# Optimization experiments

Hardware: AMD Instinct MI355X
Metric: run time of the kernel (lower is better)

The kernel has to match this reference:

```python
import jax, jax.numpy as jnp
import numpy as np

B, T, U, F, H, V = 4, 512, 96, 512, 512, 256
NEG_INF = -1e30


def setup_inputs() -> dict:
    key = jax.random.key(0)
    ks = jax.random.split(key, 7)
    frames = jax.random.normal(ks[0], (B, T, F), dtype=jnp.float32)
    # guarantee num_frames >= num_labels so a valid alignment path exists
    num_frames = jax.random.randint(ks[1], (B,), T // 2, T + 1, dtype=jnp.int32)
    labels = jax.random.randint(ks[2], (B, U), 1, V + 1, dtype=jnp.int32)
    num_labels = jax.random.randint(ks[3], (B,), U // 2, U + 1, dtype=jnp.int32)
    scale = 0.02
    Wf = scale * jax.random.normal(ks[4], (F, H), dtype=jnp.float32)
    E = scale * jax.random.normal(ks[5], (V + 1, H), dtype=jnp.float32)
    Wo = scale * jax.random.normal(ks[6], (H, V + 1), dtype=jnp.float32)
    return dict(frames=frames, num_frames=num_frames, labels=labels,
                num_labels=num_labels, Wf=Wf, E=E, Wo=Wo)


def _lattice_loss(frames, num_frames, labels, num_labels, Wf, E, Wo):
    Bd, Td, _ = frames.shape
    Ud = labels.shape[1]
    # 1-gram context dependency: context state after u emitted labels is
    # 0 (start) if u == 0 else labels[u-1].  ctx: [B, U+1]
    ctx = jnp.concatenate([jnp.zeros((Bd, 1), labels.dtype), labels], axis=1)
    # locally normalized weight fn (RNN-T style joint network)
    fproj = jnp.einsum('btf,fh->bth', frames, Wf)                 # [B,T,H]
    cemb = jnp.take(E, ctx, axis=0)                               # [B,U+1,H]
    h = jnp.tanh(fproj[:, :, None, :] + cemb[:, None, :, :])      # [B,T,U+1,H]
    logits = jax.nn.log_softmax(
        jnp.einsum('btuh,hv->btuv', h, Wo), axis=-1)              # [B,T,U+1,V+1]
    blank = logits[..., 0]                                        # [B,T,U+1]
    # lexical arc weight for emitting label u+1 from state u:
    # lex[b,t,u] = logits[b,t,u, labels[b,u]]
    idx = jnp.broadcast_to(labels[:, None, :, None].astype(jnp.int32),
                           (Bd, Td, Ud, 1))
    lex = jnp.take_along_axis(logits[:, :, :Ud, :], idx, axis=3)[..., 0]  # [B,T,U]

    # forward DP under the Log semiring over the (t, u) string lattice
    alpha0 = jnp.full((Bd, Ud + 1), NEG_INF, dtype=logits.dtype).at[:, 0].set(0.0)

    def step(alpha, xs):
        blank_t, lex_t, t = xs  # [B,U+1], [B,U], scalar
        stay = alpha + blank_t
        emit = jnp.concatenate(
            [jnp.full((Bd, 1), NEG_INF, dtype=alpha.dtype),
             alpha[:, :-1] + lex_t], axis=1)
        new = jnp.logaddexp(stay, emit)
        new = jnp.where((t < num_frames)[:, None], new, alpha)
        return new, None

    xs = (jnp.swapaxes(blank, 0, 1), jnp.swapaxes(lex, 0, 1), jnp.arange(Td))
    alpha, _ = jax.lax.scan(step, alpha0, xs)
    logp = jnp.take_along_axis(alpha, num_labels[:, None].astype(jnp.int32),
                               axis=1)[:, 0]
    return -logp  # [B] negative sequence log-probability


def reference(frames, num_frames, labels, num_labels, Wf, E, Wo):
    return _lattice_loss(frames, num_frames, labels, num_labels, Wf, E, Wo)
```

## Files before the change

### kernel.cpp

```cpp
#include <hip/hip_runtime.h>
#include <hip/hip_bf16.h>


#define BB 4
#define TT 512
#define UU 96
#define FF 512
#define HH 512
#define VV 256
#define NV (VV + 1)
#define NU (UU + 1)
#define NP 272
#define NEG_INF (-1e30f)
#define LOG2E 1.4426950408889634f
#define LN2 0.6931471805599453f
#define NG 128
#define GSTRIDE 520
#define WOSCL 64.0f
#define INVWOSCL 0.015625f
#define BCHUNK 17408
#define BLONGS 2176

typedef _Float16 f16;
typedef __attribute__((ext_vector_type(8))) _Float16 f16x8;
typedef __bf16 bf16;
typedef __bf16 bf16x8 __attribute__((ext_vector_type(8)));
typedef float f32x4 __attribute__((ext_vector_type(4)));

__device__ __forceinline__ f16x8 splat8(float s) {
    f16 v = (f16)s;
    f16x8 r = {v, v, v, v, v, v, v, v};
    return r;
}

__device__ __forceinline__ long tanh_pack8(f16x8 fv8, f16x8 cv8) {
    f16x8 x = fv8 + cv8;
    x = __builtin_elementwise_min(__builtin_elementwise_max(x, splat8(-2.0f)),
                                  splat8(2.0f));
    f16x8 y = x * x;
    f16x8 q = y * splat8(-0.0067528f) + splat8(0.0700672f);
    q = y * q + splat8(-0.301720f);
    q = y * q + splat8(1.0f);
    f16x8 t = x * q;
    int lo = 0, hi = 0;
    lo = __builtin_amdgcn_cvt_pk_fp8_f32((float)t[0], (float)t[1], lo, false);
    lo = __builtin_amdgcn_cvt_pk_fp8_f32((float)t[2], (float)t[3], lo, true);
    hi = __builtin_amdgcn_cvt_pk_fp8_f32((float)t[4], (float)t[5], hi, false);
    hi = __builtin_amdgcn_cvt_pk_fp8_f32((float)t[6], (float)t[7], hi, true);
    return (long)(((unsigned long long)(unsigned int)lo) |
                  (((unsigned long long)(unsigned int)hi) << 32));
}

__device__ __forceinline__ long pack_fp8x8(const float* v) {
    int lo = 0, hi = 0;
    lo = __builtin_amdgcn_cvt_pk_fp8_f32(v[0], v[1], lo, false);
    lo = __builtin_amdgcn_cvt_pk_fp8_f32(v[2], v[3], lo, true);
    hi = __builtin_amdgcn_cvt_pk_fp8_f32(v[4], v[5], hi, false);
    hi = __builtin_amdgcn_cvt_pk_fp8_f32(v[6], v[7], hi, true);
    return (long)(((unsigned long long)(unsigned int)lo) |
                  (((unsigned long long)(unsigned int)hi) << 32));
}

__device__ __forceinline__ float lae2(float x, float y) {
    float m = fmaxf(x, y);
    float d = fminf(x, y) - m;
    return m + __builtin_amdgcn_logf(1.0f + __builtin_amdgcn_exp2f(d));
}

__device__ __forceinline__ float lse3_2(float x, float y, float z) {
    float m = fmaxf(fmaxf(x, y), z);
    float s = __builtin_amdgcn_exp2f(x - m) + __builtin_amdgcn_exp2f(y - m) +
              __builtin_amdgcn_exp2f(z - m);
    return m + __builtin_amdgcn_logf(s);
}

__device__ __forceinline__ float lse5_2(float a, float b, float c, float d, float e) {
    float m = fmaxf(fmaxf(fmaxf(a, b), fmaxf(c, d)), e);
    float s = __builtin_amdgcn_exp2f(a - m) + __builtin_amdgcn_exp2f(b - m) +
              __builtin_amdgcn_exp2f(c - m) + __builtin_amdgcn_exp2f(d - m) +
              __builtin_amdgcn_exp2f(e - m);
    return m + __builtin_amdgcn_logf(s);
}

__device__ __forceinline__ void async_copy16(const void* g, void* l) {
    __builtin_amdgcn_global_load_lds(
        (const __attribute__((address_space(1))) unsigned int*)g,
        (__attribute__((address_space(3))) unsigned int*)l, 16, 0, 0);
}

__global__ __launch_bounds__(256, 2) void k_front(
    const float* __restrict__ frames, const float* __restrict__ Wf,
    const float* __restrict__ Wo, const float* __restrict__ E,
    const int* __restrict__ labels, f16* __restrict__ fproj,
    long* __restrict__ Wo_s, f16* __restrict__ cemb) {
    __shared__ bf16 Alds[64 * 40];
    __shared__ bf16 Blds[64 * 40];
    const int blk = blockIdx.x;
    const int tid = threadIdx.x;

    if (blk < 256) {
        const int r0 = (blk & 31) * 64;
        const int n0 = (blk >> 5) * 64;
        const int lane = tid & 63, w = tid >> 6;
        const int c = lane & 15, g = lane >> 4;

        const int srow = tid >> 2, sko = (tid & 3) * 8;
        const float* fptr = frames + (size_t)(r0 + srow) * FF + sko;
        const int q = tid >> 6, c64 = tid & 63;

        f32x4 acc[4];
#pragma unroll
        for (int j = 0; j < 4; ++j) acc[j] = (f32x4){0.f, 0.f, 0.f, 0.f};

        for (int kt = 0; kt < FF; kt += 32) {
            float4 f1 = *(const float4*)(fptr + kt);
            float4 f2 = *(const float4*)(fptr + kt + 4);
            bf16x8 av = {(bf16)f1.x, (bf16)f1.y, (bf16)f1.z, (bf16)f1.w,
                         (bf16)f2.x, (bf16)f2.y, (bf16)f2.z, (bf16)f2.w};
            *(bf16x8*)&Alds[srow * 40 + sko] = av;
#pragma unroll
            for (int p = 0; p < 8; ++p) {
                float v = Wf[(size_t)(kt + q * 8 + p) * HH + n0 + c64];
                Blds[c64 * 40 + q * 8 + p] = (bf16)v;
            }
            __syncthreads();
            const int m = w * 16;
            bf16x8 af = *(const bf16x8*)&Alds[(m + c) * 40 + g * 8];
#pragma unroll
            for (int j = 0; j < 4; ++j) {
                bf16x8 bv = *(const bf16x8*)&Blds[(j * 16 + c) * 40 + g * 8];
                acc[j] = __builtin_amdgcn_mfma_f32_16x16x32_bf16(af, bv, acc[j], 0, 0, 0);
            }
            __syncthreads();
        }
        const int m = w * 16;
#pragma unroll
        for (int j = 0; j < 4; ++j)
#pragma unroll
            for (int r = 0; r < 4; ++r)
                fproj[(size_t)(r0 + m + g * 4 + r) * HH + n0 + j * 16 + c] = (f16)acc[j][r];
    } else if (blk < 324) {
        int idx = (blk - 256) * 256 + tid;
        int n = idx % NP;
        int rest = idx / NP;
        int kg = rest & 3;
        int k32 = rest >> 2;
        float v[8];
#pragma unroll
        for (int e = 0; e < 8; ++e) {
            int k = k32 * 32 + kg * 8 + e;
            v[e] = (n < NV) ? Wo[k * NV + n] * WOSCL : 0.f;
        }
        Wo_s[idx] = pack_fp8x8(v);
    } else {
        int u = blk - 324;
        for (int b = 0; b < BB; ++b) {
            int ctx = (u == 0) ? 0 : labels[b * UU + (u - 1)];
            const float* src = E + (size_t)ctx * HH;
            f16* dst = cemb + ((size_t)b * NU + u) * HH;
            for (int i = tid; i < HH; i += 256) dst[i] = (f16)src[i];
        }
    }
}

__global__ __launch_bounds__(256, 4) void k_joint(
    const f16* __restrict__ fproj, const f16* __restrict__ cemb,
    const long* __restrict__ Wo_s, const int* __restrict__ labels,
    const int* __restrict__ num_frames, float* __restrict__ cl_arr) {
    __shared__ long B_s8[2][BLONGS];

    const int tid = threadIdx.x;
    const int b = blockIdx.y;
    const int r0 = blockIdx.x * 64;
    const int nf = num_frames[b];
    if (r0 / NU >= nf) return;

    const int lane = tid & 63, w = tid >> 6;
    const int c = lane & 15, g = lane >> 4;

    const int gr = r0 + w * 16 + c;
    const int at = gr / NU, au = gr - at * NU;
    const f16* pf = fproj + ((size_t)(b * TT + at)) * HH + g * 8;
    const f16* pc = cemb + ((size_t)(b * NU + au)) * HH + g * 8;
    const char* wsrcB = (const char*)Wo_s + lane * 16;

    f32x4 acc[17];
#pragma unroll
    for (int j = 0; j < 17; ++j) acc[j] = (f32x4){0.f, 0.f, 0.f, 0.f};

    const int bB0 = g * NP + c;

    long a0, a1;

    {
        for (int ch = w; ch < 17; ch += 4)
            async_copy16(wsrcB + ch * 1024, (char*)&B_s8[0][0] + ch * 1024 + lane * 16);
        f16x8 fv0 = *(const f16x8*)pf;
        f16x8 cv0 = *(const f16x8*)pc;
        f16x8 fv1 = *(const f16x8*)(pf + 32);
        f16x8 cv1 = *(const f16x8*)(pc + 32);
        a0 = tanh_pack8(fv0, cv0);
        a1 = tanh_pack8(fv1, cv1);
        __syncthreads();
    }

    for (int i = 0; i < 8; ++i) {
        const int cur = i & 1, nxt = cur ^ 1;
        f16x8 fv0, cv0, fv1, cv1;
        if (i < 7) {
            const char* wk = wsrcB + (size_t)(i + 1) * BCHUNK;
            for (int ch = w; ch < 17; ch += 4)
                async_copy16(wk + ch * 1024, (char*)&B_s8[nxt][0] + ch * 1024 + lane * 16);
            const int kt = (i + 1) * 64;
            fv0 = *(const f16x8*)(pf + kt);
            cv0 = *(const f16x8*)(pc + kt);
            fv1 = *(const f16x8*)(pf + kt + 32);
            cv1 = *(const f16x8*)(pc + kt + 32);
        }
        __builtin_amdgcn_s_setprio(1);
#pragma unroll
        for (int j = 0; j < 17; ++j) {
            long bv = B_s8[cur][bB0 + j * 16];
            acc[j] = __builtin_amdgcn_mfma_f32_16x16x32_fp8_fp8(a0, bv, acc[j], 0, 0, 0);
        }
        __builtin_amdgcn_s_setprio(0);
        long a0n, a1n;
        if (i < 7) {
            a0n = tanh_pack8(fv0, cv0);
            a1n = tanh_pack8(fv1, cv1);
        }
        __builtin_amdgcn_s_setprio(1);
#pragma unroll
        for (int j = 0; j < 17; ++j) {
            long bv = B_s8[cur][bB0 + 1088 + j * 16];
            acc[j] = __builtin_amdgcn_mfma_f32_16x16x32_fp8_fp8(a1, bv, acc[j], 0, 0, 0);
        }
        __builtin_amdgcn_s_setprio(0);
        if (i < 7) {
            a0 = a0n;
            a1 = a1n;
            __syncthreads();
        }
    }

#pragma unroll
    for (int j = 0; j < 17; ++j) acc[j] = acc[j] * INVWOSCL;

    const int rbase = r0 + w * 16 + g * 4;
#pragma unroll
    for (int r = 0; r < 4; ++r) {
        const int grr = rbase + r;
        const int t = grr / NU, u = grr - t * NU;

        float mx = NEG_INF;
#pragma unroll
        for (int j = 0; j < 17; ++j) {
            int col = j * 16 + c;
            if (col < NV) mx = fmaxf(mx, acc[j][r]);
        }
#pragma unroll
        for (int s = 1; s < 16; s <<= 1) mx = fmaxf(mx, __shfl_xor(mx, s));
        float sum = 0.f;
#pragma unroll
        for (int j = 0; j < 17; ++j) {
            int col = j * 16 + c;
            if (col < NV) sum += __expf(acc[j][r] - mx);
        }
#pragma unroll
        for (int s = 1; s < 16; s <<= 1) sum += __shfl_xor(sum, s);
        float lse = mx + __logf(sum);

        float blankv = __shfl(acc[0][r], lane & 48);
        int L = (u < UU) ? labels[b * UU + u] : 0;
        int jl = L >> 4;
        float v = acc[0][r];
#pragma unroll
        for (int j = 1; j < 17; ++j)
            if (jl == j) v = acc[j][r];
        float lexv = __shfl(v, (lane & 48) | (L & 15));

        if (c == 0) {
            float2 ov;
            ov.x = blankv - lse;
            ov.y = (u < UU) ? (lexv - lse) : 0.f;
            *(float2*)&cl_arr[(((size_t)b * TT + t) * NU + u) * 2] = ov;
        }
    }
}

__global__ __launch_bounds__(128) void k_compact(
    const float* __restrict__ cl, const int* __restrict__ num_frames,
    float* __restrict__ Dg) {
    const int g = blockIdx.x;
    const int b = blockIdx.y;
    const int u = threadIdx.x;
    if (u >= NU) return;
    const int nf = num_frames[b];
    const float2* P = (const float2*)(cl + (size_t)b * TT * NU * 2);

    auto fetch = [&](int t, int uu, float& bb, float& ll) {
        if (uu <= UU) {
            float2 z = P[t * NU + uu];
            bool act = t < nf;
            bb = act ? z.x * LOG2E : 0.f;
            ll = (act && uu < UU) ? z.y * LOG2E : NEG_INF;
        } else {
            bb = NEG_INF;
            ll = NEG_INF;
        }
    };

    const int t0 = g * 4;
    float b0, l0, b1u, l1u, b1u1, l1u1;
    fetch(t0, u, b0, l0);
    fetch(t0 + 1, u, b1u, l1u);
    fetch(t0 + 1, u + 1, b1u1, l1u1);
    float A0 = b0 + b1u;
    float A1 = lae2(l0 + b1u1, b0 + l1u);
    float A2 = l0 + l1u1;
    float B0[3], B1[3], B2[3];
#pragma unroll
    for (int j = 0; j < 3; ++j) {
        float b2v, l2v, b3v, l3v, b3n, l3n;
        fetch(t0 + 2, u + j, b2v, l2v);
        fetch(t0 + 3, u + j, b3v, l3v);
        fetch(t0 + 3, u + j + 1, b3n, l3n);
        B0[j] = b2v + b3v;
        B1[j] = lae2(l2v + b3n, b2v + l3v);
        B2[j] = l2v + l3n;
    }
    float* d = Dg + ((size_t)b * NG + g) * GSTRIDE;
    d[u] = A0 + B0[0];
    d[104 + u] = lae2(A1 + B0[1], A0 + B1[0]);
    d[208 + u] = lse3_2(A2 + B0[2], A1 + B1[1], A0 + B2[0]);
    d[312 + u] = lae2(A2 + B1[2], A1 + B2[1]);
    d[416 + u] = A2 + B2[2];
}

__global__ __launch_bounds__(64) void k_dpser(
    const float* __restrict__ Dg, const int* __restrict__ num_labels,
    float* __restrict__ out) {
    const int b = blockIdx.x;
    const int lane = threadIdx.x;
    const float* D = Dg + (size_t)b * NG * GSTRIDE;
    const int lo_u = lane;
    const int hi_u = 64 + ((lane < 33) ? lane : 0);

    float a_lo = (lane == 0) ? 0.f : NEG_INF;
    float a_hi = NEG_INF;

    constexpr int R = 8;
    float blo[R][5], bhi[R][5];
#pragma unroll
    for (int g = 0; g < R; ++g)
#pragma unroll
        for (int k = 0; k < 5; ++k) {
            blo[g][k] = D[g * GSTRIDE + k * 104 + lo_u];
            bhi[g][k] = D[g * GSTRIDE + k * 104 + hi_u];
        }

#pragma unroll 8
    for (int g = 0; g < NG; ++g) {
        const int slot = g & (R - 1);
        float el[5], eh[5];
#pragma unroll
        for (int k = 0; k < 5; ++k) {
            el[k] = a_lo + blo[slot][k];
            eh[k] = a_hi + bhi[slot][k];
        }
        const int gp = g + R;
        if (gp < NG) {
#pragma unroll
            for (int k = 0; k < 5; ++k) {
                blo[slot][k] = D[gp * GSTRIDE + k * 104 + lo_u];
                bhi[slot][k] = D[gp * GSTRIDE + k * 104 + hi_u];
            }
        }
        float ml[5], mh[5];
        ml[0] = el[0];
        mh[0] = eh[0];
#pragma unroll
        for (int k = 1; k < 5; ++k) {
            float su = __shfl_up(el[k], k);
            ml[k] = (lane >= k) ? su : NEG_INF;
            float sh = __shfl_up(eh[k], k);
            float xl = __shfl(el[k], 64 - k + lane);
            mh[k] = (lane >= k) ? sh : xl;
        }
        a_lo = lse5_2(ml[0], ml[1], ml[2], ml[3], ml[4]);
        float nh = lse5_2(mh[0], mh[1], mh[2], mh[3], mh[4]);
        if (lane < 33) a_hi = nh;
    }

    const int nl = num_labels[b];
    float res = (nl < 64) ? __shfl(a_lo, nl) : __shfl(a_hi, nl - 64);
    if (lane == 0) out[b] = -res * LN2;
}

extern "C" void kernel_launch(void* const* d_in, const int* in_sizes, int n_in,
                              void* d_out, int out_size, void* d_ws, size_t ws_size,
                              hipStream_t stream) {
    const float* frames = (const float*)d_in[0];
    const int* num_frames = (const int*)d_in[1];
    const int* labels = (const int*)d_in[2];
    const int* num_labels = (const int*)d_in[3];
    const float* Wf = (const float*)d_in[4];
    const float* E = (const float*)d_in[5];
    const float* Wo = (const float*)d_in[6];
    float* out = (float*)d_out;

    char* ws = (char*)d_ws;
    size_t off = 0;
    long* Wo_s = (long*)(ws + off); off += (size_t)17408 * 8;
    f16* cemb = (f16*)(ws + off); off += (size_t)BB * NU * HH * 2;
    off = (off + 255) & ~(size_t)255;
    f16* fproj = (f16*)(ws + off); off += (size_t)BB * TT * HH * 2;
    off = (off + 255) & ~(size_t)255;
    float* cl_arr = (float*)(ws + off); off += (size_t)BB * TT * NU * 2 * 4;
    off = (off + 255) & ~(size_t)255;
    float* Dg = (float*)(ws + off); off += (size_t)BB * NG * GSTRIDE * 4;

    hipLaunchKernelGGL(k_front, dim3(421), dim3(256), 0, stream,
                       frames, Wf, Wo, E, labels, fproj, Wo_s, cemb);
    hipLaunchKernelGGL(k_joint, dim3((TT * NU) / 64, BB), dim3(256), 0, stream,
                       fproj, cemb, Wo_s, labels, num_frames, cl_arr);
    hipLaunchKernelGGL(k_compact, dim3(NG, BB), dim3(128), 0, stream,
                       cl_arr, num_frames, Dg);
    hipLaunchKernelGGL(k_dpser, dim3(BB), dim3(64), 0, stream,
                       Dg, num_labels, out);
}
```

Before: 187.3 us.

## Compute the 257th vocab column with f16 dot products instead of a padded MFMA tile

The joint GEMM previously padded the vocabulary to 272 columns, spending a whole 17th MFMA column tile (mostly zeros) just to get column 256. That column is now computed per thread as an f16 fused multiply-add dot product of the tanh activations with a separately staged f16 weight column. Lane shuffles reduce it, and the result is merged into the log-softmax and the label lookup. This cuts MFMA work, LDS staging and accumulator registers by about one sixteenth, but adds VALU work and leaves that column accumulated in f16, with different precision than the fp8 MFMA path.

```diff
diff --git a/kernel.cpp b/kernel.cpp
--- a/kernel.cpp
+++ b/kernel.cpp
@@ -10,7 +10,7 @@
 #define VV 256
 #define NV (VV + 1)
 #define NU (UU + 1)
-#define NP 272
+#define NP 256
 #define NEG_INF (-1e30f)
 #define LOG2E 1.4426950408889634f
 #define LN2 0.6931471805599453f
@@ -18,8 +18,9 @@
 #define GSTRIDE 520
 #define WOSCL 64.0f
 #define INVWOSCL 0.015625f
-#define BCHUNK 17408
-#define BLONGS 2176
+#define BCHUNK 16384
+#define BLONGS 2048
+#define SPLANE 1024
 
 typedef _Float16 f16;
 typedef __attribute__((ext_vector_type(8))) _Float16 f16x8;
@@ -33,7 +34,7 @@
     return r;
 }
 
-__device__ __forceinline__ long tanh_pack8(f16x8 fv8, f16x8 cv8) {
+__device__ __forceinline__ f16x8 tanh8(f16x8 fv8, f16x8 cv8) {
     f16x8 x = fv8 + cv8;
     x = __builtin_elementwise_min(__builtin_elementwise_max(x, splat8(-2.0f)),
                                   splat8(2.0f));
@@ -41,7 +42,10 @@
     f16x8 q = y * splat8(-0.0067528f) + splat8(0.0700672f);
     q = y * q + splat8(-0.301720f);
     q = y * q + splat8(1.0f);
-    f16x8 t = x * q;
+    return x * q;
+}
+
+__device__ __forceinline__ long pack8(f16x8 t) {
     int lo = 0, hi = 0;
     lo = __builtin_amdgcn_cvt_pk_fp8_f32((float)t[0], (float)t[1], lo, false);
     lo = __builtin_amdgcn_cvt_pk_fp8_f32((float)t[2], (float)t[3], lo, true);
@@ -92,7 +96,7 @@
     const float* __restrict__ frames, const float* __restrict__ Wf,
     const float* __restrict__ Wo, const float* __restrict__ E,
     const int* __restrict__ labels, f16* __restrict__ fproj,
-    long* __restrict__ Wo_s, f16* __restrict__ cemb) {
+    long* __restrict__ Wo_s, f16* __restrict__ wcol, f16* __restrict__ cemb) {
     __shared__ bf16 Alds[64 * 40];
     __shared__ bf16 Blds[64 * 40];
     const int blk = blockIdx.x;
@@ -139,21 +143,23 @@
 #pragma unroll
             for (int r = 0; r < 4; ++r)
                 fproj[(size_t)(r0 + m + g * 4 + r) * HH + n0 + j * 16 + c] = (f16)acc[j][r];
-    } else if (blk < 324) {
+    } else if (blk < 320) {
         int idx = (blk - 256) * 256 + tid;
-        int n = idx % NP;
-        int rest = idx / NP;
+        int n = idx & 255;
+        int rest = idx >> 8;
         int kg = rest & 3;
         int k32 = rest >> 2;
         float v[8];
 #pragma unroll
         for (int e = 0; e < 8; ++e) {
             int k = k32 * 32 + kg * 8 + e;
-            v[e] = (n < NV) ? Wo[k * NV + n] * WOSCL : 0.f;
+            v[e] = Wo[k * NV + n] * WOSCL;
         }
         Wo_s[idx] = pack_fp8x8(v);
+    } else if (blk == 320) {
+        for (int k = tid; k < HH; k += 256) wcol[k] = (f16)Wo[k * NV + 256];
     } else {
-        int u = blk - 324;
+        int u = blk - 321;
         for (int b = 0; b < BB; ++b) {
             int ctx = (u == 0) ? 0 : labels[b * UU + (u - 1)];
             const float* src = E + (size_t)ctx * HH;
@@ -165,8 +171,9 @@
 
 __global__ __launch_bounds__(256, 4) void k_joint(
     const f16* __restrict__ fproj, const f16* __restrict__ cemb,
-    const long* __restrict__ Wo_s, const int* __restrict__ labels,
-    const int* __restrict__ num_frames, float* __restrict__ cl_arr) {
+    const long* __restrict__ Wo_s, const f16* __restrict__ wcol,
+    const int* __restrict__ labels, const int* __restrict__ num_frames,
+    float* __restrict__ cl_arr) {
     __shared__ long B_s8[2][BLONGS];
 
     const int tid = threadIdx.x;
@@ -182,57 +189,71 @@
     const int at = gr / NU, au = gr - at * NU;
     const f16* pf = fproj + ((size_t)(b * TT + at)) * HH + g * 8;
     const f16* pc = cemb + ((size_t)(b * NU + au)) * HH + g * 8;
+    const f16* wc = wcol + g * 8;
     const char* wsrcB = (const char*)Wo_s + lane * 16;
 
-    f32x4 acc[17];
-#pragma unroll
-    for (int j = 0; j < 17; ++j) acc[j] = (f32x4){0.f, 0.f, 0.f, 0.f};
+    f32x4 acc[16];
+#pragma unroll
+    for (int j = 0; j < 16; ++j) acc[j] = (f32x4){0.f, 0.f, 0.f, 0.f};
 
     const int bB0 = g * NP + c;
 
     long a0, a1;
+    f16x8 c256h;
 
     {
-        for (int ch = w; ch < 17; ch += 4)
+        for (int ch = w; ch < 16; ch += 4)
             async_copy16(wsrcB + ch * 1024, (char*)&B_s8[0][0] + ch * 1024 + lane * 16);
         f16x8 fv0 = *(const f16x8*)pf;
         f16x8 cv0 = *(const f16x8*)pc;
         f16x8 fv1 = *(const f16x8*)(pf + 32);
         f16x8 cv1 = *(const f16x8*)(pc + 32);
-        a0 = tanh_pack8(fv0, cv0);
-        a1 = tanh_pack8(fv1, cv1);
+        f16x8 wv0 = *(const f16x8*)wc;
+        f16x8 wv1 = *(const f16x8*)(wc + 32);
+        f16x8 t0 = tanh8(fv0, cv0);
+        f16x8 t1 = tanh8(fv1, cv1);
+        c256h = t0 * wv0;
+        c256h = t1 * wv1 + c256h;
+        a0 = pack8(t0);
+        a1 = pack8(t1);
         __syncthreads();
     }
 
     for (int i = 0; i < 8; ++i) {
         const int cur = i & 1, nxt = cur ^ 1;
-        f16x8 fv0, cv0, fv1, cv1;
+        f16x8 fv0, cv0, fv1, cv1, wv0, wv1;
         if (i < 7) {
             const char* wk = wsrcB + (size_t)(i + 1) * BCHUNK;
-            for (int ch = w; ch < 17; ch += 4)
+            for (int ch = w; ch < 16; ch += 4)
                 async_copy16(wk + ch * 1024, (char*)&B_s8[nxt][0] + ch * 1024 + lane * 16);
             const int kt = (i + 1) * 64;
             fv0 = *(const f16x8*)(pf + kt);
             cv0 = *(const f16x8*)(pc + kt);
             fv1 = *(const f16x8*)(pf + kt + 32);
             cv1 = *(const f16x8*)(pc + kt + 32);
+            wv0 = *(const f16x8*)(wc + kt);
+            wv1 = *(const f16x8*)(wc + kt + 32);
         }
         __builtin_amdgcn_s_setprio(1);
 #pragma unroll
-        for (int j = 0; j < 17; ++j) {
+        for (int j = 0; j < 16; ++j) {
             long bv = B_s8[cur][bB0 + j * 16];
             acc[j] = __builtin_amdgcn_mfma_f32_16x16x32_fp8_fp8(a0, bv, acc[j], 0, 0, 0);
         }
         __builtin_amdgcn_s_setprio(0);
         long a0n, a1n;
         if (i < 7) {
-            a0n = tanh_pack8(fv0, cv0);
-            a1n = tanh_pack8(fv1, cv1);
+            f16x8 t0 = tanh8(fv0, cv0);
+            f16x8 t1 = tanh8(fv1, cv1);
+            c256h = t0 * wv0 + c256h;
+            c256h = t1 * wv1 + c256h;
+            a0n = pack8(t0);
+            a1n = pack8(t1);
         }
         __builtin_amdgcn_s_setprio(1);
 #pragma unroll
-        for (int j = 0; j < 17; ++j) {
-            long bv = B_s8[cur][bB0 + 1088 + j * 16];
+        for (int j = 0; j < 16; ++j) {
+            long bv = B_s8[cur][bB0 + SPLANE + j * 16];
             acc[j] = __builtin_amdgcn_mfma_f32_16x16x32_fp8_fp8(a1, bv, acc[j], 0, 0, 0);
         }
         __builtin_amdgcn_s_setprio(0);
@@ -244,7 +265,14 @@
     }
 
 #pragma unroll
-    for (int j = 0; j < 17; ++j) acc[j] = acc[j] * INVWOSCL;
+    for (int j = 0; j < 16; ++j) acc[j] = acc[j] * INVWOSCL;
+
+    float c256 = ((float)c256h[0] + (float)c256h[1]) +
+                 ((float)c256h[2] + (float)c256h[3]) +
+                 ((float)c256h[4] + (float)c256h[5]) +
+                 ((float)c256h[6] + (float)c256h[7]);
+    c256 += __shfl_xor(c256, 16);
+    c256 += __shfl_xor(c256, 32);
 
     const int rbase = r0 + w * 16 + g * 4;
 #pragma unroll
@@ -252,22 +280,20 @@
         const int grr = rbase + r;
         const int t = grr / NU, u = grr - t * NU;
 
+        float c256v = __shfl(c256, (lane & 48) | ((g * 4 + r) & 15));
+
         float mx = NEG_INF;
 #pragma unroll
-        for (int j = 0; j < 17; ++j) {
-            int col = j * 16 + c;
-            if (col < NV) mx = fmaxf(mx, acc[j][r]);
-        }
+        for (int j = 0; j < 16; ++j) mx = fmaxf(mx, acc[j][r]);
 #pragma unroll
         for (int s = 1; s < 16; s <<= 1) mx = fmaxf(mx, __shfl_xor(mx, s));
+        mx = fmaxf(mx, c256v);
         float sum = 0.f;
 #pragma unroll
-        for (int j = 0; j < 17; ++j) {
-            int col = j * 16 + c;
-            if (col < NV) sum += __expf(acc[j][r] - mx);
-        }
+        for (int j = 0; j < 16; ++j) sum += __expf(acc[j][r] - mx);
 #pragma unroll
         for (int s = 1; s < 16; s <<= 1) sum += __shfl_xor(sum, s);
+        sum += __expf(c256v - mx);
         float lse = mx + __logf(sum);
 
         float blankv = __shfl(acc[0][r], lane & 48);
@@ -275,9 +301,10 @@
         int jl = L >> 4;
         float v = acc[0][r];
 #pragma unroll
-        for (int j = 1; j < 17; ++j)
+        for (int j = 1; j < 16; ++j)
             if (jl == j) v = acc[j][r];
         float lexv = __shfl(v, (lane & 48) | (L & 15));
+        if (jl == 16) lexv = c256v;
 
         if (c == 0) {
             float2 ov;
@@ -411,7 +438,8 @@
 
     char* ws = (char*)d_ws;
     size_t off = 0;
-    long* Wo_s = (long*)(ws + off); off += (size_t)17408 * 8;
+    long* Wo_s = (long*)(ws + off); off += (size_t)16384 * 8;
+    f16* wcol = (f16*)(ws + off); off += (size_t)HH * 2;
     f16* cemb = (f16*)(ws + off); off += (size_t)BB * NU * HH * 2;
     off = (off + 255) & ~(size_t)255;
     f16* fproj = (f16*)(ws + off); off += (size_t)BB * TT * HH * 2;
@@ -420,10 +448,10 @@
     off = (off + 255) & ~(size_t)255;
     float* Dg = (float*)(ws + off); off += (size_t)BB * NG * GSTRIDE * 4;
 
-    hipLaunchKernelGGL(k_front, dim3(421), dim3(256), 0, stream,
-                       frames, Wf, Wo, E, labels, fproj, Wo_s, cemb);
+    hipLaunchKernelGGL(k_front, dim3(418), dim3(256), 0, stream,
+                       frames, Wf, Wo, E, labels, fproj, Wo_s, wcol, cemb);
     hipLaunchKernelGGL(k_joint, dim3((TT * NU) / 64, BB), dim3(256), 0, stream,
-                       fproj, cemb, Wo_s, labels, num_frames, cl_arr);
+                       fproj, cemb, Wo_s, wcol, labels, num_frames, cl_arr);
     hipLaunchKernelGGL(k_compact, dim3(NG, BB), dim3(128), 0, stream,
                        cl_arr, num_frames, Dg);
     hipLaunchKernelGGL(k_dpser, dim3(BB), dim3(64), 0, stream,
```

After: 188.1 us. About the same (+0.4%).

## Prefetch activation operands two K-steps ahead with partial vmcnt barriers

Applied to the files above, without the earlier changes.

The joint GEMM loop now loads the fproj/cemb fp16 slices two iterations ahead into a double-buffered register set, where before it loaded only one ahead. Full __syncthreads is replaced by s_waitcnt vmcnt(4) plus s_barrier, so the barrier waits only on the async LDS weight copies and not on the in-flight register prefetches. The loop is fully unrolled and launch bounds drop from 4 to 3 waves per SIMD, giving the extra live registers room. The trade is lower occupancy and a hand-counted vmcnt that must match the number of outstanding loads exactly.

```diff
diff --git a/kernel.cpp b/kernel.cpp
--- a/kernel.cpp
+++ b/kernel.cpp
@@ -20,6 +20,7 @@
 #define INVWOSCL 0.015625f
 #define BCHUNK 17408
 #define BLONGS 2176
+#define SPLANE 1088
 
 typedef _Float16 f16;
 typedef __attribute__((ext_vector_type(8))) _Float16 f16x8;
@@ -33,7 +34,7 @@
     return r;
 }
 
-__device__ __forceinline__ long tanh_pack8(f16x8 fv8, f16x8 cv8) {
+__device__ __forceinline__ f16x8 tanh8(f16x8 fv8, f16x8 cv8) {
     f16x8 x = fv8 + cv8;
     x = __builtin_elementwise_min(__builtin_elementwise_max(x, splat8(-2.0f)),
                                   splat8(2.0f));
@@ -41,7 +42,10 @@
     f16x8 q = y * splat8(-0.0067528f) + splat8(0.0700672f);
     q = y * q + splat8(-0.301720f);
     q = y * q + splat8(1.0f);
-    f16x8 t = x * q;
+    return x * q;
+}
+
+__device__ __forceinline__ long pack8(f16x8 t) {
     int lo = 0, hi = 0;
     lo = __builtin_amdgcn_cvt_pk_fp8_f32((float)t[0], (float)t[1], lo, false);
     lo = __builtin_amdgcn_cvt_pk_fp8_f32((float)t[2], (float)t[3], lo, true);
@@ -86,6 +90,15 @@
     __builtin_amdgcn_global_load_lds(
         (const __attribute__((address_space(1))) unsigned int*)g,
         (__attribute__((address_space(3))) unsigned int*)l, 16, 0, 0);
+}
+
+__device__ __forceinline__ void bar_vm4() {
+    asm volatile("s_waitcnt vmcnt(4)" ::: "memory");
+    __builtin_amdgcn_s_barrier();
+}
+__device__ __forceinline__ void bar_vm0() {
+    asm volatile("s_waitcnt vmcnt(0)" ::: "memory");
+    __builtin_amdgcn_s_barrier();
 }
 
 __global__ __launch_bounds__(256, 2) void k_front(
@@ -163,7 +176,7 @@
     }
 }
 
-__global__ __launch_bounds__(256, 4) void k_joint(
+__global__ __launch_bounds__(256, 3) void k_joint(
     const f16* __restrict__ fproj, const f16* __restrict__ cemb,
     const long* __restrict__ Wo_s, const int* __restrict__ labels,
     const int* __restrict__ num_frames, float* __restrict__ cl_arr) {
@@ -191,31 +204,38 @@
     const int bB0 = g * NP + c;
 
     long a0, a1;
+    f16x8 Lf[2][2], Lc[2][2];
 
     {
         for (int ch = w; ch < 17; ch += 4)
             async_copy16(wsrcB + ch * 1024, (char*)&B_s8[0][0] + ch * 1024 + lane * 16);
-        f16x8 fv0 = *(const f16x8*)pf;
-        f16x8 cv0 = *(const f16x8*)pc;
-        f16x8 fv1 = *(const f16x8*)(pf + 32);
-        f16x8 cv1 = *(const f16x8*)(pc + 32);
-        a0 = tanh_pack8(fv0, cv0);
-        a1 = tanh_pack8(fv1, cv1);
-        __syncthreads();
-    }
-
+        f16x8 p0 = *(const f16x8*)pf;
+        f16x8 q0 = *(const f16x8*)pc;
+        f16x8 p1 = *(const f16x8*)(pf + 32);
+        f16x8 q1 = *(const f16x8*)(pc + 32);
+        Lf[1][0] = *(const f16x8*)(pf + 64);
+        Lc[1][0] = *(const f16x8*)(pc + 64);
+        Lf[1][1] = *(const f16x8*)(pf + 96);
+        Lc[1][1] = *(const f16x8*)(pc + 96);
+        a0 = pack8(tanh8(p0, q0));
+        a1 = pack8(tanh8(p1, q1));
+        bar_vm4();
+    }
+
+#pragma unroll
     for (int i = 0; i < 8; ++i) {
         const int cur = i & 1, nxt = cur ^ 1;
-        f16x8 fv0, cv0, fv1, cv1;
         if (i < 7) {
             const char* wk = wsrcB + (size_t)(i + 1) * BCHUNK;
             for (int ch = w; ch < 17; ch += 4)
                 async_copy16(wk + ch * 1024, (char*)&B_s8[nxt][0] + ch * 1024 + lane * 16);
-            const int kt = (i + 1) * 64;
-            fv0 = *(const f16x8*)(pf + kt);
-            cv0 = *(const f16x8*)(pc + kt);
-            fv1 = *(const f16x8*)(pf + kt + 32);
-            cv1 = *(const f16x8*)(pc + kt + 32);
+        }
+        if (i < 6) {
+            const int kt = (i + 2) * 64;
+            Lf[i & 1][0] = *(const f16x8*)(pf + kt);
+            Lc[i & 1][0] = *(const f16x8*)(pc + kt);
+            Lf[i & 1][1] = *(const f16x8*)(pf + kt + 32);
+            Lc[i & 1][1] = *(const f16x8*)(pc + kt + 32);
         }
         __builtin_amdgcn_s_setprio(1);
 #pragma unroll
@@ -226,20 +246,23 @@
         __builtin_amdgcn_s_setprio(0);
         long a0n, a1n;
         if (i < 7) {
-            a0n = tanh_pack8(fv0, cv0);
-            a1n = tanh_pack8(fv1, cv1);
+            f16x8 t0 = tanh8(Lf[(i + 1) & 1][0], Lc[(i + 1) & 1][0]);
+            f16x8 t1 = tanh8(Lf[(i + 1) & 1][1], Lc[(i + 1) & 1][1]);
+            a0n = pack8(t0);
+            a1n = pack8(t1);
         }
         __builtin_amdgcn_s_setprio(1);
 #pragma unroll
         for (int j = 0; j < 17; ++j) {
-            long bv = B_s8[cur][bB0 + 1088 + j * 16];
+            long bv = B_s8[cur][bB0 + SPLANE + j * 16];
             acc[j] = __builtin_amdgcn_mfma_f32_16x16x32_fp8_fp8(a1, bv, acc[j], 0, 0, 0);
         }
         __builtin_amdgcn_s_setprio(0);
         if (i < 7) {
             a0 = a0n;
             a1 = a1n;
-            __syncthreads();
+            if (i < 6) bar_vm4();
+            else       bar_vm0();
         }
     }
 
```

Result: no change. 190.6 us (+1.8%).
